# Optimization experiments

Measured on AMD Instinct MI355X. Metric: run time of the kernel, lower is better.

The kernel has to match this reference:

```python
import jax, jax.numpy as jnp
import numpy as np


def setup_inputs() -> dict:
    key = jax.random.key(0)
    k1, k2 = jax.random.split(key)
    n_nodes, d_feat, n_edges = 100000, 48, 1600000
    x = jax.random.normal(k1, (n_nodes, d_feat), dtype=jnp.float32)
    edge_index = jax.random.randint(k2, (2, n_edges), 0, n_nodes, dtype=jnp.int64)
    return {"x": x, "edge_index": edge_index, "batch_size": 65536}


def reference(x, edge_index, batch_size):
    # adj = SparseTensor.from_edge_index(edge_index): adj[row, col] = 1 with
    # row = edge_index[0] (src), col = edge_index[1] (dst).
    # adj.t() @ x  ->  out[i] = sum over edges (src -> i) of x[src]
    src, dst = edge_index[0], edge_index[1]
    n_nodes = x.shape[0]
    # memory-bound gather + scatter-add (SpMM, sum aggregation)
    x_neighbors_sum = jax.ops.segment_sum(x[src], dst, num_segments=n_nodes)
    node_labels = jnp.concatenate(
        (x[:batch_size, :], x_neighbors_sum[:batch_size, :]), axis=-1
    )
    return node_labels
```

## Files before the change

kernel.cpp:

```cpp
#include <hip/hip_runtime.h>
#include <hip/hip_fp16.h>

#define DFEAT 48
#define OUTW  96
#define NBINB 512
#define BINTH 512
#define EPT   7
#define SORTCAP 3328
#define NBUCK2 512
#define RBITS 7
#define NROWS 128
#define RAWCAP 2560
#define HCAP 1536


static __device__ __forceinline__ unsigned short f2h(float f) {
    __half h = __float2half_rn(f);
    return *reinterpret_cast<unsigned short*>(&h);
}
static __device__ __forceinline__ float h2f(unsigned short u) {
    __half_raw hr; hr.x = u;
    return __half2float(*reinterpret_cast<__half*>(&hr));
}

__global__ __launch_bounds__(BINTH)
void bin_k(const int* __restrict__ ei, int n_edges, int batch, int chunk,
           const float4* __restrict__ x4, int nx4, uint2* __restrict__ xh4,
           unsigned short* __restrict__ starts, unsigned int* __restrict__ regions,
           int use_half) {
    __shared__ int cnt[NBUCK2];
    __shared__ int cur[NBUCK2];
    __shared__ unsigned int sorted[SORTCAP];
    const int t = threadIdx.x;
    const int b = blockIdx.x;

    if (use_half) {
        for (int i = b * BINTH + t; i < nx4; i += NBINB * BINTH) {
            float4 v = x4[i];
            unsigned short h0 = f2h(v.x), h1 = f2h(v.y);
            unsigned short h2 = f2h(v.z), h3 = f2h(v.w);
            xh4[i] = make_uint2((unsigned)h0 | ((unsigned)h1 << 16),
                                (unsigned)h2 | ((unsigned)h3 << 16));
        }
    }

    const int beg = b * chunk;
    const int end = min(beg + chunk, n_edges);

    unsigned int pay[EPT];
    int bkt[EPT];
    #pragma unroll
    for (int i = 0; i < EPT; i++) {
        bkt[i] = -1;
        int e = beg + t + i * BINTH;
        if (e < end) {
            int dst = ei[n_edges + e];
            if (dst < batch) {
                int src = ei[e];
                bkt[i] = dst >> RBITS;
                pay[i] = ((unsigned)(dst & (NROWS - 1)) << 17) | (unsigned)src;
            }
        }
    }
    cnt[t] = 0;
    __syncthreads();
    #pragma unroll
    for (int i = 0; i < EPT; i++)
        if (bkt[i] >= 0) atomicAdd(&cnt[bkt[i]], 1);
    __syncthreads();
    int v = cnt[t];
    cur[t] = v;
    __syncthreads();
    for (int d = 1; d < NBUCK2; d <<= 1) {
        int tv = (t >= d) ? cur[t - d] : 0;
        __syncthreads();
        cur[t] += tv;
        __syncthreads();
    }
    int tot  = cur[NBUCK2 - 1];
    int excl = cur[t] - v;
    __syncthreads();
    cur[t] = excl;
    starts[t * NBINB + b] = (unsigned short)excl;
    if (t == 0) starts[NBUCK2 * NBINB + b] = (unsigned short)tot;
    __syncthreads();
    #pragma unroll
    for (int i = 0; i < EPT; i++)
        if (bkt[i] >= 0) {
            int pos = atomicAdd(&cur[bkt[i]], 1);
            sorted[pos] = pay[i];
        }
    __syncthreads();
    unsigned int* reg = regions + (size_t)b * chunk;
    for (int i = t; i < tot; i += BINTH) reg[i] = sorted[i];
}

__global__ __launch_bounds__(512)
void reduce_k(const float* __restrict__ x, const unsigned short* __restrict__ xh,
              const unsigned short* __restrict__ starts,
              const unsigned int* __restrict__ regions,
              float* __restrict__ out, int batch, int chunk, int use_half) {
    __shared__ unsigned int raw[RAWCAP];
    __shared__ int csr[HCAP];
    __shared__ int rs[NBINB], rp[NBINB], rl[NBINB];
    __shared__ int cnt[64], off[65], cur[64];
    const int t = threadIdx.x;
    const int kb = blockIdx.x >> 1;
    const int half = blockIdx.x & 1;

    {
        int s0 = starts[kb * NBINB + t];
        int s1 = starts[(kb + 1) * NBINB + t];
        rs[t] = s0; rl[t] = s1 - s0; rp[t] = s1 - s0;
    }
    __syncthreads();
    for (int d = 1; d < NBINB; d <<= 1) {
        int tv = (t >= d) ? rp[t - d] : 0;
        __syncthreads();
        rp[t] += tv;
        __syncthreads();
    }
    const int T = min(rp[NBINB - 1], RAWCAP);
    const int base = rp[t] - rl[t];
    __syncthreads();
    {
        int len = rl[t];
        const unsigned int* reg = regions + (size_t)t * chunk + rs[t];
        for (int i = 0; i < len; i++) {
            int p = base + i;
            if (p < RAWCAP) raw[p] = reg[i];
        }
    }
    __syncthreads();
    if (t < 64) cnt[t] = 0;
    __syncthreads();
    for (int i = t; i < T; i += 512) {
        int rw = raw[i] >> 17;
        if ((rw >> 6) == half) atomicAdd(&cnt[rw & 63], 1);
    }
    __syncthreads();
    int v = (t < 64) ? cnt[t] : 0;
    if (t < 64) off[t] = v;
    __syncthreads();
    for (int d = 1; d < 64; d <<= 1) {
        int tv = (t < 64 && t >= d) ? off[t - d] : 0;
        __syncthreads();
        if (t < 64) off[t] += tv;
        __syncthreads();
    }
    if (t == 63) off[64] = off[63];
    int excl = (t < 64) ? off[t] - v : 0;
    __syncthreads();
    if (t < 64) { off[t] = excl; cur[t] = excl; }
    __syncthreads();
    for (int i = t; i < T; i += 512) {
        unsigned int p = raw[i];
        int rw = p >> 17;
        if ((rw >> 6) == half) {
            int pos = atomicAdd(&cur[rw & 63], 1);
            if (pos < HCAP) csr[pos] = (int)(p & 0x1FFFFu);
        }
    }
    __syncthreads();
    const int wave = t >> 6, lane = t & 63;
    if (lane < DFEAT) {
        for (int r = wave; r < 64; r += 8) {
            int row = kb * NROWS + half * 64 + r;
            if (row >= batch) break;
            int s0 = off[r], s1 = min(off[r + 1], HCAP);
            float acc = 0.f;
            int e = s0;
            if (use_half) {
                for (; e + 4 <= s1; e += 4) {
                    float v0 = h2f(xh[(size_t)csr[e + 0] * DFEAT + lane]);
                    float v1 = h2f(xh[(size_t)csr[e + 1] * DFEAT + lane]);
                    float v2 = h2f(xh[(size_t)csr[e + 2] * DFEAT + lane]);
                    float v3 = h2f(xh[(size_t)csr[e + 3] * DFEAT + lane]);
                    acc += v0 + v1 + v2 + v3;
                }
                for (; e < s1; ++e)
                    acc += h2f(xh[(size_t)csr[e] * DFEAT + lane]);
            } else {
                for (; e + 4 <= s1; e += 4) {
                    float v0 = x[(size_t)csr[e + 0] * DFEAT + lane];
                    float v1 = x[(size_t)csr[e + 1] * DFEAT + lane];
                    float v2 = x[(size_t)csr[e + 2] * DFEAT + lane];
                    float v3 = x[(size_t)csr[e + 3] * DFEAT + lane];
                    acc += v0 + v1 + v2 + v3;
                }
                for (; e < s1; ++e)
                    acc += x[(size_t)csr[e] * DFEAT + lane];
            }
            out[(size_t)row * OUTW + lane]         = x[(size_t)row * DFEAT + lane];
            out[(size_t)row * OUTW + DFEAT + lane] = acc;
        }
    }
}


#define D4   12
#define ROW4 24

__global__ void init_out_kernel(const float4* __restrict__ x4,
                                float4* __restrict__ out4, int batch) {
    int idx = blockIdx.x * blockDim.x + threadIdx.x;
    int total = batch * ROW4;
    if (idx >= total) return;
    int row = idx / ROW4;
    int c   = idx - row * ROW4;
    float4 v;
    if (c < D4) v = x4[row * D4 + c];
    else        v = make_float4(0.f, 0.f, 0.f, 0.f);
    out4[idx] = v;
}

__global__ void scatter_edges_kernel(const float4* __restrict__ x4,
                                     const int* __restrict__ ei,
                                     float* __restrict__ out,
                                     int n_edges, int batch) {
    int tid = blockIdx.x * blockDim.x + threadIdx.x;
    int e = tid / D4;
    int q = tid - e * D4;
    if (e >= n_edges) return;
    int dst = ei[n_edges + e];
    if (dst >= batch) return;
    int src = ei[e];
    float4 v = x4[src * D4 + q];
    float* p = out + (size_t)dst * OUTW + DFEAT + q * 4;
    atomicAdd(p + 0, v.x);
    atomicAdd(p + 1, v.y);
    atomicAdd(p + 2, v.z);
    atomicAdd(p + 3, v.w);
}


extern "C" void kernel_launch(void* const* d_in, const int* in_sizes, int n_in,
                              void* d_out, int out_size, void* d_ws, size_t ws_size,
                              hipStream_t stream) {
    const float* x  = (const float*)d_in[0];
    const int*   ei = (const int*)d_in[1];
    float* out = (float*)d_out;

    const int n_edges = in_sizes[1] / 2;
    const int batch   = out_size / OUTW;
    const int n_nodes = in_sizes[0] / DFEAT;
    const int chunk   = (n_edges + NBINB - 1) / NBINB;
    const int nbuck   = (batch + NROWS - 1) / NROWS;
    const int nx4     = n_nodes * DFEAT / 4;

    size_t xh_bytes = ((size_t)n_nodes * DFEAT * sizeof(unsigned short) + 15) & ~(size_t)15;
    size_t starts_bytes = (size_t)(NBUCK2 + 1) * NBINB * sizeof(unsigned short);
    size_t reg_bytes = (size_t)NBINB * chunk * sizeof(unsigned int);
    size_t need_h = xh_bytes + starts_bytes + reg_bytes;
    size_t need_f = starts_bytes + reg_bytes;

    bool base_ok = chunk <= SORTCAP && chunk <= BINTH * EPT &&
                   n_nodes <= (1 << 17) && batch <= NBUCK2 * NROWS &&
                   (n_nodes * DFEAT) % 4 == 0 && nbuck >= 1;

    if (base_ok && ws_size >= need_h) {
        unsigned short* xh = (unsigned short*)d_ws;
        unsigned short* starts = (unsigned short*)((char*)d_ws + xh_bytes);
        unsigned int* regions = (unsigned int*)((char*)d_ws + xh_bytes + starts_bytes);
        bin_k<<<NBINB, BINTH, 0, stream>>>(ei, n_edges, batch, chunk,
                                           (const float4*)x, nx4, (uint2*)xh,
                                           starts, regions, 1);
        reduce_k<<<nbuck * 2, 512, 0, stream>>>(x, xh, starts, regions, out,
                                                batch, chunk, 1);
    } else if (base_ok && ws_size >= need_f) {
        unsigned short* starts = (unsigned short*)d_ws;
        unsigned int* regions = (unsigned int*)((char*)d_ws + starts_bytes);
        bin_k<<<NBINB, BINTH, 0, stream>>>(ei, n_edges, batch, chunk,
                                           (const float4*)x, nx4, (uint2*)0,
                                           starts, regions, 0);
        reduce_k<<<nbuck * 2, 512, 0, stream>>>(x, (const unsigned short*)0,
                                                starts, regions, out,
                                                batch, chunk, 0);
    } else {
        {
            int total = batch * ROW4;
            int grid = (total + 255) / 256;
            init_out_kernel<<<grid, 256, 0, stream>>>((const float4*)x,
                                                      (float4*)out, batch);
        }
        {
            long long total = (long long)n_edges * D4;
            long long grid = (total + 255) / 256;
            scatter_edges_kernel<<<(int)grid, 256, 0, stream>>>(
                (const float4*)x, ei, out, n_edges, batch);
        }
    }
}
```

Measured before the change: 127.3 us.

## Merge reduce halves into 1024-thread blocks, shuffle scans, vectorized half gathers

Replaces the shared-memory Hillis-Steele scans in both kernels with wave-shuffle scans, which removes many block barriers. Each reduce block now covers all 128 rows with 1024 threads instead of two 512-thread blocks that each re-load the same raw region and handle 64 rows. The fp16 gather loads 8-byte chunks (4 halves) per lane, with 4 edges processed per wave step, and combines the partial sums with cross-lane shuffles. It also writes the output with float4 stores. Halving the grid lowers block-level parallelism, and larger shared buffers may reduce occupancy.

```diff
diff --git a/kernel.cpp b/kernel.cpp
--- a/kernel.cpp
+++ b/kernel.cpp
@@ -6,21 +6,26 @@
 #define NBINB 512
 #define BINTH 512
 #define EPT   7
-#define SORTCAP 3328
+#define SORTCAP 3584
 #define NBUCK2 512
 #define RBITS 7
 #define NROWS 128
 #define RAWCAP 2560
-#define HCAP 1536
+#define CSRCAP 2560
 
 
 static __device__ __forceinline__ unsigned short f2h(float f) {
     __half h = __float2half_rn(f);
     return *reinterpret_cast<unsigned short*>(&h);
 }
-static __device__ __forceinline__ float h2f(unsigned short u) {
-    __half_raw hr; hr.x = u;
-    return __half2float(*reinterpret_cast<__half*>(&hr));
+
+static __device__ __forceinline__ int wave_iscan(int v, int lane) {
+    #pragma unroll
+    for (int d = 1; d < 64; d <<= 1) {
+        int tv = __shfl_up(v, d, 64);
+        if (lane >= d) v += tv;
+    }
+    return v;
 }
 
 __global__ __launch_bounds__(BINTH)
@@ -30,17 +35,18 @@
            int use_half) {
     __shared__ int cnt[NBUCK2];
     __shared__ int cur[NBUCK2];
+    __shared__ int wsum[BINTH / 64];
+    __shared__ int totS;
     __shared__ unsigned int sorted[SORTCAP];
     const int t = threadIdx.x;
     const int b = blockIdx.x;
+    const int lane = t & 63, wid = t >> 6;
 
     if (use_half) {
         for (int i = b * BINTH + t; i < nx4; i += NBINB * BINTH) {
             float4 v = x4[i];
-            unsigned short h0 = f2h(v.x), h1 = f2h(v.y);
-            unsigned short h2 = f2h(v.z), h3 = f2h(v.w);
-            xh4[i] = make_uint2((unsigned)h0 | ((unsigned)h1 << 16),
-                                (unsigned)h2 | ((unsigned)h3 << 16));
+            xh4[i] = make_uint2((unsigned)f2h(v.x) | ((unsigned)f2h(v.y) << 16),
+                                (unsigned)f2h(v.z) | ((unsigned)f2h(v.w) << 16));
         }
     }
 
@@ -69,17 +75,18 @@
         if (bkt[i] >= 0) atomicAdd(&cnt[bkt[i]], 1);
     __syncthreads();
     int v = cnt[t];
-    cur[t] = v;
-    __syncthreads();
-    for (int d = 1; d < NBUCK2; d <<= 1) {
-        int tv = (t >= d) ? cur[t - d] : 0;
-        __syncthreads();
-        cur[t] += tv;
-        __syncthreads();
-    }
-    int tot  = cur[NBUCK2 - 1];
-    int excl = cur[t] - v;
-    __syncthreads();
+    int iv = wave_iscan(v, lane);
+    if (lane == 63) wsum[wid] = iv;
+    __syncthreads();
+    if (t < BINTH / 64) {
+        int wv = wsum[t];
+        int sv = wave_iscan(wv, t);
+        wsum[t] = sv - wv;
+        if (t == BINTH / 64 - 1) totS = sv;
+    }
+    __syncthreads();
+    int excl = iv - v + wsum[wid];
+    int tot = totS;
     cur[t] = excl;
     starts[t * NBINB + b] = (unsigned short)excl;
     if (t == 0) starts[NBUCK2 * NBINB + b] = (unsigned short)tot;
@@ -95,104 +102,124 @@
     for (int i = t; i < tot; i += BINTH) reg[i] = sorted[i];
 }
 
-__global__ __launch_bounds__(512)
-void reduce_k(const float* __restrict__ x, const unsigned short* __restrict__ xh,
+__global__ __launch_bounds__(1024)
+void reduce_k(const float* __restrict__ x, const uint2* __restrict__ xh2,
               const unsigned short* __restrict__ starts,
               const unsigned int* __restrict__ regions,
               float* __restrict__ out, int batch, int chunk, int use_half) {
     __shared__ unsigned int raw[RAWCAP];
-    __shared__ int csr[HCAP];
-    __shared__ int rs[NBINB], rp[NBINB], rl[NBINB];
-    __shared__ int cnt[64], off[65], cur[64];
+    __shared__ int csr[CSRCAP];
+    __shared__ int cnt[NROWS], off[NROWS + 1], cur[NROWS];
+    __shared__ int wsum[16];
+    __shared__ int totS;
     const int t = threadIdx.x;
-    const int kb = blockIdx.x >> 1;
-    const int half = blockIdx.x & 1;
-
-    {
-        int s0 = starts[kb * NBINB + t];
+    const int kb = blockIdx.x;
+    const int lane = t & 63, wid = t >> 6;
+
+    int s0 = 0, len = 0;
+    if (t < NBINB) {
+        s0 = starts[kb * NBINB + t];
         int s1 = starts[(kb + 1) * NBINB + t];
-        rs[t] = s0; rl[t] = s1 - s0; rp[t] = s1 - s0;
-    }
-    __syncthreads();
-    for (int d = 1; d < NBINB; d <<= 1) {
-        int tv = (t >= d) ? rp[t - d] : 0;
-        __syncthreads();
-        rp[t] += tv;
-        __syncthreads();
-    }
-    const int T = min(rp[NBINB - 1], RAWCAP);
-    const int base = rp[t] - rl[t];
-    __syncthreads();
-    {
-        int len = rl[t];
-        const unsigned int* reg = regions + (size_t)t * chunk + rs[t];
+        len = s1 - s0;
+    }
+    int iv = wave_iscan(len, lane);
+    if (lane == 63 && wid < 8) wsum[wid] = iv;
+    __syncthreads();
+    if (t < 8) {
+        int wv = wsum[t];
+        int sv = wave_iscan(wv, t);
+        wsum[t] = sv - wv;
+        if (t == 7) totS = sv;
+    }
+    __syncthreads();
+    const int T = min(totS, RAWCAP);
+    if (t < NBINB && len > 0) {
+        int base = iv - len + wsum[wid];
+        const unsigned int* reg = regions + (size_t)t * chunk + s0;
         for (int i = 0; i < len; i++) {
             int p = base + i;
             if (p < RAWCAP) raw[p] = reg[i];
         }
     }
-    __syncthreads();
-    if (t < 64) cnt[t] = 0;
-    __syncthreads();
-    for (int i = t; i < T; i += 512) {
-        int rw = raw[i] >> 17;
-        if ((rw >> 6) == half) atomicAdd(&cnt[rw & 63], 1);
-    }
-    __syncthreads();
-    int v = (t < 64) ? cnt[t] : 0;
-    if (t < 64) off[t] = v;
-    __syncthreads();
-    for (int d = 1; d < 64; d <<= 1) {
-        int tv = (t < 64 && t >= d) ? off[t - d] : 0;
-        __syncthreads();
-        if (t < 64) off[t] += tv;
-        __syncthreads();
-    }
-    if (t == 63) off[64] = off[63];
-    int excl = (t < 64) ? off[t] - v : 0;
-    __syncthreads();
-    if (t < 64) { off[t] = excl; cur[t] = excl; }
-    __syncthreads();
-    for (int i = t; i < T; i += 512) {
+    if (t < NROWS) cnt[t] = 0;
+    __syncthreads();
+    for (int i = t; i < T; i += 1024) atomicAdd(&cnt[raw[i] >> 17], 1);
+    __syncthreads();
+    int v2 = (t < NROWS) ? cnt[t] : 0;
+    int iv2 = wave_iscan(v2, lane);
+    if (lane == 63 && wid < 2) wsum[wid] = iv2;
+    __syncthreads();
+    if (t == 0) {
+        int a = wsum[0];
+        off[NROWS] = a + wsum[1];
+        wsum[1] = a;
+        wsum[0] = 0;
+    }
+    __syncthreads();
+    if (t < NROWS) {
+        int excl = iv2 - v2 + wsum[wid];
+        off[t] = excl;
+        cur[t] = excl;
+    }
+    __syncthreads();
+    for (int i = t; i < T; i += 1024) {
         unsigned int p = raw[i];
-        int rw = p >> 17;
-        if ((rw >> 6) == half) {
-            int pos = atomicAdd(&cur[rw & 63], 1);
-            if (pos < HCAP) csr[pos] = (int)(p & 0x1FFFFu);
-        }
-    }
-    __syncthreads();
-    const int wave = t >> 6, lane = t & 63;
-    if (lane < DFEAT) {
-        for (int r = wave; r < 64; r += 8) {
-            int row = kb * NROWS + half * 64 + r;
+        int pos = atomicAdd(&cur[p >> 17], 1);
+        if (pos < CSRCAP) csr[pos] = (int)(p & 0x1FFFFu);
+    }
+    __syncthreads();
+
+    if (use_half) {
+        const int g  = lane / 12;
+        const int cg = lane - g * 12;
+        const bool act = lane < 48;
+        const float4* x4 = (const float4*)x;
+        float4* out4 = (float4*)out;
+        for (int r = wid; r < NROWS; r += 16) {
+            int row = kb * NROWS + r;
             if (row >= batch) break;
-            int s0 = off[r], s1 = min(off[r + 1], HCAP);
-            float acc = 0.f;
-            int e = s0;
-            if (use_half) {
-                for (; e + 4 <= s1; e += 4) {
-                    float v0 = h2f(xh[(size_t)csr[e + 0] * DFEAT + lane]);
-                    float v1 = h2f(xh[(size_t)csr[e + 1] * DFEAT + lane]);
-                    float v2 = h2f(xh[(size_t)csr[e + 2] * DFEAT + lane]);
-                    float v3 = h2f(xh[(size_t)csr[e + 3] * DFEAT + lane]);
-                    acc += v0 + v1 + v2 + v3;
+            int e0 = off[r], e1 = min(off[r + 1], CSRCAP);
+            float4 acc = make_float4(0.f, 0.f, 0.f, 0.f);
+            for (int eb = e0; eb < e1; eb += 8) {
+                int ea = eb + g;
+                int ebn = eb + 4 + g;
+                if (act && ea < e1) {
+                    uint2 p = xh2[(size_t)csr[ea] * 12 + cg];
+                    float2 f0 = __half22float2(*(const __half2*)&p.x);
+                    float2 f1 = __half22float2(*(const __half2*)&p.y);
+                    acc.x += f0.x; acc.y += f0.y; acc.z += f1.x; acc.w += f1.y;
                 }
-                for (; e < s1; ++e)
-                    acc += h2f(xh[(size_t)csr[e] * DFEAT + lane]);
-            } else {
-                for (; e + 4 <= s1; e += 4) {
-                    float v0 = x[(size_t)csr[e + 0] * DFEAT + lane];
-                    float v1 = x[(size_t)csr[e + 1] * DFEAT + lane];
-                    float v2 = x[(size_t)csr[e + 2] * DFEAT + lane];
-                    float v3 = x[(size_t)csr[e + 3] * DFEAT + lane];
-                    acc += v0 + v1 + v2 + v3;
+                if (act && ebn < e1) {
+                    uint2 p = xh2[(size_t)csr[ebn] * 12 + cg];
+                    float2 f0 = __half22float2(*(const __half2*)&p.x);
+                    float2 f1 = __half22float2(*(const __half2*)&p.y);
+                    acc.x += f0.x; acc.y += f0.y; acc.z += f1.x; acc.w += f1.y;
                 }
-                for (; e < s1; ++e)
+            }
+            float4 bb;
+            bb.x = __shfl(acc.x, lane + 24); bb.y = __shfl(acc.y, lane + 24);
+            bb.z = __shfl(acc.z, lane + 24); bb.w = __shfl(acc.w, lane + 24);
+            if (lane < 24) { acc.x += bb.x; acc.y += bb.y; acc.z += bb.z; acc.w += bb.w; }
+            bb.x = __shfl(acc.x, lane + 12); bb.y = __shfl(acc.y, lane + 12);
+            bb.z = __shfl(acc.z, lane + 12); bb.w = __shfl(acc.w, lane + 12);
+            if (lane < 12) {
+                acc.x += bb.x; acc.y += bb.y; acc.z += bb.z; acc.w += bb.w;
+                out4[(size_t)row * 24 + 12 + cg] = acc;
+                out4[(size_t)row * 24 + cg] = x4[(size_t)row * 12 + cg];
+            }
+        }
+    } else {
+        if (lane < DFEAT) {
+            for (int r = wid; r < NROWS; r += 16) {
+                int row = kb * NROWS + r;
+                if (row >= batch) break;
+                int e0 = off[r], e1 = min(off[r + 1], CSRCAP);
+                float acc = 0.f;
+                for (int e = e0; e < e1; ++e)
                     acc += x[(size_t)csr[e] * DFEAT + lane];
+                out[(size_t)row * OUTW + lane]         = x[(size_t)row * DFEAT + lane];
+                out[(size_t)row * OUTW + DFEAT + lane] = acc;
             }
-            out[(size_t)row * OUTW + lane]         = x[(size_t)row * DFEAT + lane];
-            out[(size_t)row * OUTW + DFEAT + lane] = acc;
         }
     }
 }
@@ -256,7 +283,7 @@
 
     bool base_ok = chunk <= SORTCAP && chunk <= BINTH * EPT &&
                    n_nodes <= (1 << 17) && batch <= NBUCK2 * NROWS &&
-                   (n_nodes * DFEAT) % 4 == 0 && nbuck >= 1;
+                   (n_nodes * DFEAT) % 4 == 0 && nbuck >= 1 && nbuck <= NBUCK2;
 
     if (base_ok && ws_size >= need_h) {
         unsigned short* xh = (unsigned short*)d_ws;
@@ -265,17 +292,16 @@
         bin_k<<<NBINB, BINTH, 0, stream>>>(ei, n_edges, batch, chunk,
                                            (const float4*)x, nx4, (uint2*)xh,
                                            starts, regions, 1);
-        reduce_k<<<nbuck * 2, 512, 0, stream>>>(x, xh, starts, regions, out,
-                                                batch, chunk, 1);
+        reduce_k<<<nbuck, 1024, 0, stream>>>(x, (const uint2*)xh, starts, regions,
+                                             out, batch, chunk, 1);
     } else if (base_ok && ws_size >= need_f) {
         unsigned short* starts = (unsigned short*)d_ws;
         unsigned int* regions = (unsigned int*)((char*)d_ws + starts_bytes);
         bin_k<<<NBINB, BINTH, 0, stream>>>(ei, n_edges, batch, chunk,
                                            (const float4*)x, nx4, (uint2*)0,
                                            starts, regions, 0);
-        reduce_k<<<nbuck * 2, 512, 0, stream>>>(x, (const unsigned short*)0,
-                                                starts, regions, out,
-                                                batch, chunk, 0);
+        reduce_k<<<nbuck, 1024, 0, stream>>>(x, (const uint2*)0, starts, regions,
+                                             out, batch, chunk, 0);
     } else {
         {
             int total = batch * ROW4;
```

After: 122.8 us. -3.5%, faster.
